# Optimization experiments

Measured on AMD Instinct MI355X. Metric: run time of the kernel, lower is better.

## Reference

```python
import jax, jax.numpy as jnp
import numpy as np

B, S, D = 4, 1024, 1024
H, HD = 16, 64
MAXPOS = 1024  # max_position_embeddings


def setup_inputs() -> dict:
    key = jax.random.key(0)
    ks = jax.random.split(key, 10)
    sc = 0.02
    return {
        "hidden_states": jax.random.normal(ks[0], (B, S, D), dtype=jnp.float32),
        "attention_mask": jnp.zeros((B, 1, 1, S), dtype=jnp.float32),
        "across_attention_prior": jax.random.uniform(ks[1], (B, H, S, S), dtype=jnp.float32),
        "head_mask": jnp.ones((1, H, 1, 1), dtype=jnp.float32),
        "Wq": jax.random.normal(ks[2], (D, D), dtype=jnp.float32) * sc,
        "bq": jnp.zeros((D,), dtype=jnp.float32),
        "Wk": jax.random.normal(ks[3], (D, D), dtype=jnp.float32) * sc,
        "bk": jnp.zeros((D,), dtype=jnp.float32),
        "Wv": jax.random.normal(ks[4], (D, D), dtype=jnp.float32) * sc,
        "bv": jnp.zeros((D,), dtype=jnp.float32),
        "dist_emb": jax.random.normal(ks[5], (2 * MAXPOS - 1, HD), dtype=jnp.float32) * sc,
    }


def _heads(x):
    # [B,S,D] -> [B,H,S,HD]
    return x.reshape(B, S, H, HD).transpose(0, 2, 1, 3)


def reference(hidden_states, attention_mask, across_attention_prior, head_mask,
              Wq, bq, Wk, bk, Wv, bv, dist_emb):
    q = _heads(hidden_states @ Wq + bq)  # [B,H,S,HD]
    k = _heads(hidden_states @ Wk + bk)
    v = _heads(hidden_states @ Wv + bv)

    scores = jnp.einsum("bhld,bhrd->bhlr", q, k)

    # relative_key_query positional bias
    pos = jnp.arange(S)
    distance = pos[:, None] - pos[None, :]  # [S,S]
    pe = dist_emb[distance + MAXPOS - 1]  # [S,S,HD] (l, r, d)
    scores = scores + jnp.einsum("bhld,lrd->bhlr", q, pe)
    scores = scores + jnp.einsum("bhrd,lrd->bhlr", k, pe)

    scores = scores / jnp.sqrt(jnp.float32(HD))
    scores = scores + attention_mask  # additive mask, broadcast [B,1,1,S]

    probs = jax.nn.softmax(scores, axis=-1)
    probs = probs * across_attention_prior  # post-softmax multiplicative prior
    probs = probs * head_mask  # dropout prob = 0 (eval)

    ctx = jnp.einsum("bhlr,bhrd->bhld", probs, v)
    ctx = ctx.transpose(0, 2, 1, 3).reshape(B, S, D)
    return ctx
```

## Files before the change

kernel.cpp:

```cpp
#include <hip/hip_runtime.h>


typedef unsigned short u16;
typedef unsigned int   u32;
typedef unsigned long long u64;
typedef __attribute__((ext_vector_type(8))) short bfx8;
typedef __attribute__((ext_vector_type(4))) float f32x4;

#define MFMA_BF16(a, b, c) __builtin_amdgcn_mfma_f32_16x16x32_bf16(a, b, c, 0, 0, 0)

__device__ __forceinline__ u16 f2bf(float f) {
    union { float f; u32 u; } c; c.f = f;
    u32 u = c.u;
    return (u16)((u + 0x7FFFu + ((u >> 16) & 1u)) >> 16);
}
__device__ __forceinline__ float bf2f(u16 v) {
    union { u32 u; float f; } c; c.u = ((u32)v) << 16;
    return c.f;
}
__device__ __forceinline__ float load_f(const void* p, long i, bool bf) {
    return bf ? bf2f(((const u16*)p)[i]) : ((const float*)p)[i];
}
__device__ __forceinline__ u16 load_bf(const void* p, long i, bool bf) {
    return bf ? ((const u16*)p)[i] : f2bf(((const float*)p)[i]);
}

__device__ __forceinline__ void gload16(const u16* g, u16* l) {
    __builtin_amdgcn_global_load_lds(
        (__attribute__((address_space(1))) void*)g,
        (__attribute__((address_space(3))) void*)l, 16, 0, 0);
}

__device__ __forceinline__ bfx8 ld_sw(const u16* arr, int row, int chunk) {
    return *(const bfx8*)(arr + row * 64 + ((chunk ^ (row & 7)) * 8));
}

__global__ void k_detect(const u32* hid, int* flags) {
    __shared__ int cnt;
    if (threadIdx.x == 0) cnt = 0;
    __syncthreads();
    int c = 0;
    for (int i = threadIdx.x; i < 1024; i += 256) {
        u32 w = hid[i];
        u32 e = (w >> 7) & 0xFFu;
        if (e >= 100u && e <= 140u) c++;
    }
    atomicAdd(&cnt, c);
    __syncthreads();
    if (threadIdx.x == 0) flags[0] = (cnt > 512) ? 1 : 0;
}

__global__ void k_prep(const void* hidden, const void* dist, const void* mask,
                       const void* hm, const void* bq, const void* bk,
                       const void* bv, const int* flags, u16* hid_bf,
                       u16* dist_bf, float* mask_f, float* hm_f, float* bias_f) {
    const bool bf = flags[0] != 0;
    const long NH = 4L * 1024 * 1024, ND = 2047L * 64, NM = 4096, NB = 3072, NHM = 16;
    const long TOT = NH + ND + NM + NB + NHM;
    for (long i = (long)blockIdx.x * 256 + threadIdx.x; i < TOT;
         i += (long)gridDim.x * 256) {
        if (i < NH) hid_bf[i] = load_bf(hidden, i, bf);
        else if (i < NH + ND) dist_bf[i - NH] = load_bf(dist, i - NH, bf);
        else if (i < NH + ND + NM) mask_f[i - NH - ND] = load_f(mask, i - NH - ND, bf);
        else if (i < NH + ND + NM + NB) {
            long j = i - NH - ND - NM;
            const void* src = (j < 1024) ? bq : ((j < 2048) ? bk : bv);
            bias_f[j] = load_f(src, j & 1023, bf);
        } else {
            long j = i - NH - ND - NM - NB;
            hm_f[j] = load_f(hm, j, bf);
        }
    }
}

__global__ void k_transpose(const void* Wq, const void* Wk, const void* Wv,
                            const int* flags, u16* wt) {
    const bool bf = flags[0] != 0;
    __shared__ float t[32][33];
    const int z = blockIdx.z;
    const void* W = (z == 0) ? Wq : ((z == 1) ? Wk : Wv);
    int x = blockIdx.x * 32 + threadIdx.x;
    for (int i = 0; i < 4; i++) {
        int y = blockIdx.y * 32 + threadIdx.y + i * 8;
        t[threadIdx.y + i * 8][threadIdx.x] = load_f(W, (long)y * 1024 + x, bf);
    }
    __syncthreads();
    int x2 = blockIdx.y * 32 + threadIdx.x;
    u16* out = wt + (long)z * 1024 * 1024;
    for (int i = 0; i < 4; i++) {
        int y2 = blockIdx.x * 32 + threadIdx.y + i * 8;
        out[(long)y2 * 1024 + x2] = f2bf(t[threadIdx.x][threadIdx.y + i * 8]);
    }
}

__global__ __launch_bounds__(256, 2)
void k_qkv_gemm(const u16* A, const u16* Bt, const float* bias,
                u16* qb, u16* kb, u16* vb) {
    __shared__ u16 sA[128 * 32];
    __shared__ u16 sB[128 * 32];
    const int tid = threadIdx.x;
    const int w = tid >> 6, lane = tid & 63;
    const int quad = lane >> 4, nl = lane & 15;
    const int wr = w >> 1, wc = w & 1;
    const int n0 = blockIdx.x * 128, m0 = blockIdx.y * 128;

    f32x4 acc[4][4];
#pragma unroll
    for (int a = 0; a < 4; a++)
#pragma unroll
        for (int b = 0; b < 4; b++) acc[a][b] = (f32x4){0.f, 0.f, 0.f, 0.f};

    for (int kt = 0; kt < 32; kt++) {
        const int k0 = kt * 32;
        __syncthreads();
#pragma unroll
        for (int j = 0; j < 2; j++) {
            int row = 32 * w + 16 * j + (lane >> 2);
            int seg = lane & 3;
            gload16(A + (long)(m0 + row) * 1024 + k0 + seg * 8, sA + 1024 * w + 512 * j);
            gload16(Bt + (long)(n0 + row) * 1024 + k0 + seg * 8, sB + 1024 * w + 512 * j);
        }
        __syncthreads();

        bfx8 af[4], bfr[4];
#pragma unroll
        for (int f = 0; f < 4; f++) {
            af[f]  = *(const bfx8*)(sA + (64 * wr + 16 * f + nl) * 32 + quad * 8);
            bfr[f] = *(const bfx8*)(sB + (64 * wc + 16 * f + nl) * 32 + quad * 8);
        }
#pragma unroll
        for (int fm = 0; fm < 4; fm++)
#pragma unroll
            for (int fn = 0; fn < 4; fn++)
                acc[fm][fn] = MFMA_BF16(af[fm], bfr[fn], acc[fm][fn]);
    }

#pragma unroll
    for (int fm = 0; fm < 4; fm++) {
#pragma unroll
        for (int fn = 0; fn < 4; fn++) {
            int n = n0 + 64 * wc + 16 * fn + nl;
            int which = n >> 10, hcol = n & 1023;
            int h = hcol >> 6, hd = hcol & 63;
            float bias_v = bias[n];
            int mbase = m0 + 64 * wr + 16 * fm + 4 * quad;
            int b = mbase >> 10, s = mbase & 1023;
            if (which == 2) {
                u64 pk = 0;
#pragma unroll
                for (int reg = 0; reg < 4; reg++)
                    pk |= (u64)f2bf(acc[fm][fn][reg] + bias_v) << (16 * reg);
                *(u64*)&vb[((long)((b * 16 + h) * 64 + hd)) * 1024 + s] = pk;
            } else {
                u16* op = (which == 0) ? qb : kb;
#pragma unroll
                for (int reg = 0; reg < 4; reg++)
                    op[((long)((b * 16 + h) * 1024 + s + reg)) * 64 + hd] =
                        f2bf(acc[fm][fn][reg] + bias_v);
            }
        }
    }
}

__global__ __launch_bounds__(256, 3)
void k_attn(const u16* qb, const u16* kb, const u16* vTb, const u16* Eb,
            const float* maskf, const float* hmf, const void* prior,
            const int* flags, void* out) {
    __shared__ __align__(16) u16 smem[25088];
    u16* sK  = smem;
    u16* sVT = smem + 4096;
    u16* sE  = smem + 8192;
    u16* sP  = smem + 8192;
    u16* bqB = smem + 16384;
    u16* bkB = smem + 20736;

    const int tid = threadIdx.x;
    const int w = tid >> 6, lane = tid & 63;
    const int quad = lane >> 4, nl = lane & 15;
    const int rloc = lane >> 3;
    const int cperm = (lane & 7) ^ rloc;
    const int bh = blockIdx.x, b = bh >> 4, h = bh & 15;
    const int l0 = blockIdx.y * 64;
    const bool bf = flags[0] != 0;

    const u16* qbh = qb  + (long)bh * 65536;
    const u16* kbh = kb  + (long)bh * 65536;
    const u16* vbh = vTb + (long)bh * 65536;

    const bfx8 aq0 = *(const bfx8*)(qbh + (l0 + 16 * w + nl) * 64 + quad * 8);
    const bfx8 aq1 = *(const bfx8*)(qbh + (l0 + 16 * w + nl) * 64 + quad * 8 + 32);

    f32x4 accv[4];
#pragma unroll
    for (int f = 0; f < 4; f++) accv[f] = (f32x4){0.f, 0.f, 0.f, 0.f};
    float zacc[4] = {0.f, 0.f, 0.f, 0.f};
    const int jb_base = l0 + 960;

    const int lpb   = 16 * w + 4 * quad;
    const int bqrd  = lpb * 68 + 63 - nl;
    const int bkrd  = lpb * 68 + nl;

    for (int it = 0; it < 16; it++) {
        const int r0 = it * 64;
        __syncthreads();

        const int jb = jb_base - r0;
#pragma unroll
        for (int j = 0; j < 2; j++) {
            int row = 16 * w + 8 * j + rloc;
            gload16(kbh + (r0 + row) * 64 + cperm * 8, sK + (16 * w + 8 * j) * 64);
            gload16(vbh + row * 1024 + r0 + cperm * 8, sVT + (16 * w + 8 * j) * 64);
        }
#pragma unroll
        for (int j = 0; j < 4; j++) {
            int row = 32 * w + 8 * j + rloc;
            int je = jb + row;
            if (je > 2046) je = 2046;
            if (je < 0) je = 0;
            gload16(Eb + je * 64 + cperm * 8, sE + (32 * w + 8 * j) * 64);
        }
        float pr[4][4], mval[4];
#pragma unroll
        for (int fn = 0; fn < 4; fn++) {
            mval[fn] = maskf[b * 1024 + r0 + fn * 16 + nl];
#pragma unroll
            for (int reg = 0; reg < 4; reg++) {
                long pidx = ((long)(bh * 1024 + l0 + 16 * w + 4 * quad + reg)) * 1024
                            + r0 + fn * 16 + nl;
                pr[fn][reg] = bf ? bf2f(((const u16*)prior)[pidx])
                                 : ((const float*)prior)[pidx];
            }
        }
        __syncthreads();

        const bfx8 ak0 = ld_sw(sK, 16 * w + nl, quad);
        const bfx8 ak1 = ld_sw(sK, 16 * w + nl, 4 + quad);
#pragma unroll
        for (int d = 0; d < 5; d++) {
            const int fc = w + d;
            bfx8 be0 = ld_sw(sE, fc * 16 + nl, quad);
            bfx8 be1 = ld_sw(sE, fc * 16 + nl, 4 + quad);
            f32x4 dq = (f32x4){0.f, 0.f, 0.f, 0.f};
            dq = MFMA_BF16(aq0, be0, dq);
            dq = MFMA_BF16(aq1, be1, dq);
#pragma unroll
            for (int reg = 0; reg < 4; reg++) {
                int lp = lpb + reg;
                int t = 16 * fc + nl - lp;
                if (t >= 0 && t < 64) bqB[lp * 68 + t] = f2bf(dq[reg]);
            }
        }
#pragma unroll
        for (int d = 0; d < 5; d++) {
            const int fc = 3 - w + d;
            bfx8 be0 = ld_sw(sE, fc * 16 + nl, quad);
            bfx8 be1 = ld_sw(sE, fc * 16 + nl, 4 + quad);
            f32x4 dk = (f32x4){0.f, 0.f, 0.f, 0.f};
            dk = MFMA_BF16(ak0, be0, dk);
            dk = MFMA_BF16(ak1, be1, dk);
#pragma unroll
            for (int reg = 0; reg < 4; reg++) {
                int rp = lpb + reg;
                int row = 16 * fc + nl + rp - 63;
                if (row >= 0 && row < 64) bkB[row * 68 + rp] = f2bf(dk[reg]);
            }
        }
        f32x4 accs[4];
#pragma unroll
        for (int fn = 0; fn < 4; fn++) {
            bfx8 bk0 = ld_sw(sK, fn * 16 + nl, quad);
            bfx8 bk1 = ld_sw(sK, fn * 16 + nl, 4 + quad);
            f32x4 s = (f32x4){0.f, 0.f, 0.f, 0.f};
            s = MFMA_BF16(aq0, bk0, s);
            s = MFMA_BF16(aq1, bk1, s);
            accs[fn] = s;
        }
        __syncthreads();

#pragma unroll
        for (int fn = 0; fn < 4; fn++) {
#pragma unroll
            for (int reg = 0; reg < 4; reg++) {
                float dqv = bf2f(bqB[bqrd + reg * 68 - fn * 16]);
                float dkv = bf2f(bkB[bkrd + reg * 68 + fn * 16]);
                float s = (accs[fn][reg] + dqv + dkv) * 0.125f + mval[fn];
                float e = __expf(s);
                zacc[reg] += e;
                sP[(lpb + reg) * 72 + fn * 16 + nl] = f2bf(e * pr[fn][reg]);
            }
        }
        bfx8 ap0 = *(const bfx8*)(sP + (16 * w + nl) * 72 + quad * 8);
        bfx8 ap1 = *(const bfx8*)(sP + (16 * w + nl) * 72 + quad * 8 + 32);
#pragma unroll
        for (int fd = 0; fd < 4; fd++) {
            bfx8 bv0 = ld_sw(sVT, fd * 16 + nl, quad);
            bfx8 bv1 = ld_sw(sVT, fd * 16 + nl, 4 + quad);
            accv[fd] = MFMA_BF16(ap0, bv0, accv[fd]);
            accv[fd] = MFMA_BF16(ap1, bv1, accv[fd]);
        }
    }

#pragma unroll
    for (int reg = 0; reg < 4; reg++) {
        float z = zacc[reg];
        z += __shfl_xor(z, 1);
        z += __shfl_xor(z, 2);
        z += __shfl_xor(z, 4);
        z += __shfl_xor(z, 8);
        zacc[reg] = z;
    }
    const float hm = hmf[h];
#pragma unroll
    for (int fd = 0; fd < 4; fd++) {
#pragma unroll
        for (int reg = 0; reg < 4; reg++) {
            int l = l0 + 16 * w + 4 * quad + reg;
            int d = fd * 16 + nl;
            float val = accv[fd][reg] * hm / zacc[reg];
            long oidx = ((long)(b * 1024 + l)) * 1024 + h * 64 + d;
            if (bf) ((u16*)out)[oidx] = f2bf(val);
            else    ((float*)out)[oidx] = val;
        }
    }
}

extern "C" void kernel_launch(void* const* d_in, const int* in_sizes, int n_in,
                              void* d_out, int out_size, void* d_ws, size_t ws_size,
                              hipStream_t stream) {
    char* ws = (char*)d_ws;
    int*   flags   = (int*)ws;
    u16*   hid_bf  = (u16*)(ws + 256);
    u16*   wt_bf   = (u16*)(ws + 8388864);
    u16*   dist_bf = (u16*)(ws + 14680320);
    float* mask_f  = (float*)(ws + 14942464);
    float* bias_f  = (float*)(ws + 14958848);
    float* hm_f    = (float*)(ws + 14971136);
    u16*   q_bf    = (u16*)(ws + 14971392);
    u16*   k_bf    = (u16*)(ws + 23360000);
    u16*   v_bf    = (u16*)(ws + 31748608);

    k_detect<<<1, 256, 0, stream>>>((const u32*)d_in[0], flags);
    k_prep<<<2048, 256, 0, stream>>>(d_in[0], d_in[10], d_in[1], d_in[3],
                                     d_in[5], d_in[7], d_in[9], flags,
                                     hid_bf, dist_bf, mask_f, hm_f, bias_f);
    k_transpose<<<dim3(32, 32, 3), dim3(32, 8), 0, stream>>>(
        d_in[4], d_in[6], d_in[8], flags, wt_bf);
    k_qkv_gemm<<<dim3(24, 32), 256, 0, stream>>>(hid_bf, wt_bf, bias_f,
                                                 q_bf, k_bf, v_bf);
    k_attn<<<dim3(64, 16), 256, 0, stream>>>(q_bf, k_bf, v_bf, dist_bf,
                                             mask_f, hm_f, d_in[2], flags, d_out);
}
```

Before: 521.9 us.

## Prefetch prior tiles one iteration ahead and stage K/V/E through registers

The attention kernel now loads the next iteration's prior and mask values into registers while the current tile is processed, so the large prior stream is meant to overlap with compute. K, V and E tiles are loaded into registers and stored to padded LDS rows (stride 72) in place of global_load_lds with XOR swizzle, and raw s_waitcnt+s_barrier sequences replace __syncthreads. The prep kernel converts hidden states and the distance table four elements per thread with vector loads and launches half as many blocks. The cost is higher register pressure from the doubled prior buffers and staging registers, which may reduce occupancy under launch bounds of 3 blocks per CU.

```diff
diff --git a/kernel.cpp b/kernel.cpp
--- a/kernel.cpp
+++ b/kernel.cpp
@@ -9,6 +9,9 @@
 
 #define MFMA_BF16(a, b, c) __builtin_amdgcn_mfma_f32_16x16x32_bf16(a, b, c, 0, 0, 0)
 
+#define BAR_LDS() asm volatile("s_waitcnt lgkmcnt(0)\n\ts_barrier" ::: "memory")
+#define CFENCE()  asm volatile("" ::: "memory")
+
 __device__ __forceinline__ u16 f2bf(float f) {
     union { float f; u32 u; } c; c.f = f;
     u32 u = c.u;
@@ -29,10 +32,6 @@
     __builtin_amdgcn_global_load_lds(
         (__attribute__((address_space(1))) void*)g,
         (__attribute__((address_space(3))) void*)l, 16, 0, 0);
-}
-
-__device__ __forceinline__ bfx8 ld_sw(const u16* arr, int row, int chunk) {
-    return *(const bfx8*)(arr + row * 64 + ((chunk ^ (row & 7)) * 8));
 }
 
 __global__ void k_detect(const u32* hid, int* flags) {
@@ -55,20 +54,32 @@
                        const void* bv, const int* flags, u16* hid_bf,
                        u16* dist_bf, float* mask_f, float* hm_f, float* bias_f) {
     const bool bf = flags[0] != 0;
-    const long NH = 4L * 1024 * 1024, ND = 2047L * 64, NM = 4096, NB = 3072, NHM = 16;
-    const long TOT = NH + ND + NM + NB + NHM;
+    const long VH = 1048576, VD = 32752;
+    const long SC = 4096 + 3072 + 16;
+    const long TOT = VH + VD + SC;
     for (long i = (long)blockIdx.x * 256 + threadIdx.x; i < TOT;
          i += (long)gridDim.x * 256) {
-        if (i < NH) hid_bf[i] = load_bf(hidden, i, bf);
-        else if (i < NH + ND) dist_bf[i - NH] = load_bf(dist, i - NH, bf);
-        else if (i < NH + ND + NM) mask_f[i - NH - ND] = load_f(mask, i - NH - ND, bf);
-        else if (i < NH + ND + NM + NB) {
-            long j = i - NH - ND - NM;
-            const void* src = (j < 1024) ? bq : ((j < 2048) ? bk : bv);
-            bias_f[j] = load_f(src, j & 1023, bf);
+        if (i < VH + VD) {
+            const void* src = (i < VH) ? hidden : dist;
+            u16* dst = (i < VH) ? hid_bf : dist_bf;
+            long j = (i < VH) ? i : i - VH;
+            if (bf) {
+                ((int2*)dst)[j] = ((const int2*)src)[j];
+            } else {
+                float4 v = ((const float4*)src)[j];
+                ushort4 o;
+                o.x = f2bf(v.x); o.y = f2bf(v.y);
+                o.z = f2bf(v.z); o.w = f2bf(v.w);
+                ((ushort4*)dst)[j] = o;
+            }
         } else {
-            long j = i - NH - ND - NM - NB;
-            hm_f[j] = load_f(hm, j, bf);
+            long j = i - VH - VD;
+            if (j < 4096) mask_f[j] = load_f(mask, j, bf);
+            else if (j < 7168) {
+                long k = j - 4096;
+                const void* src = (k < 1024) ? bq : ((k < 2048) ? bk : bv);
+                bias_f[k] = load_f(src, k & 1023, bf);
+            } else hm_f[j - 7168] = load_f(hm, j - 7168, bf);
         }
     }
 }
@@ -166,19 +177,17 @@
 void k_attn(const u16* qb, const u16* kb, const u16* vTb, const u16* Eb,
             const float* maskf, const float* hmf, const void* prior,
             const int* flags, void* out) {
-    __shared__ __align__(16) u16 smem[25088];
+    __shared__ __align__(16) u16 smem[27136];
     u16* sK  = smem;
-    u16* sVT = smem + 4096;
-    u16* sE  = smem + 8192;
-    u16* sP  = smem + 8192;
-    u16* bqB = smem + 16384;
-    u16* bkB = smem + 20736;
+    u16* sVT = smem + 4608;
+    u16* sE  = smem + 9216;
+    u16* sP  = smem + 9216;
+    u16* bqB = smem + 18432;
+    u16* bkB = smem + 22784;
 
     const int tid = threadIdx.x;
     const int w = tid >> 6, lane = tid & 63;
     const int quad = lane >> 4, nl = lane & 15;
-    const int rloc = lane >> 3;
-    const int cperm = (lane & 7) ^ rloc;
     const int bh = blockIdx.x, b = bh >> 4, h = bh & 15;
     const int l0 = blockIdx.y * 64;
     const bool bf = flags[0] != 0;
@@ -196,50 +205,79 @@
     float zacc[4] = {0.f, 0.f, 0.f, 0.f};
     const int jb_base = l0 + 960;
 
-    const int lpb   = 16 * w + 4 * quad;
-    const int bqrd  = lpb * 68 + 63 - nl;
-    const int bkrd  = lpb * 68 + nl;
-
+    const int lpb  = 16 * w + 4 * quad;
+    const int bqrd = lpb * 68 + 63 - nl;
+    const int bkrd = lpb * 68 + nl;
+
+    float pr_c[4][4], mv_c[4], pr_n[4][4], mv_n[4];
+#pragma unroll
+    for (int fn = 0; fn < 4; fn++) {
+        mv_c[fn] = maskf[b * 1024 + fn * 16 + nl];
+#pragma unroll
+        for (int reg = 0; reg < 4; reg++) {
+            long pidx = ((long)(bh * 1024 + l0 + lpb + reg)) * 1024 + fn * 16 + nl;
+            pr_c[fn][reg] = bf ? bf2f(((const u16*)prior)[pidx])
+                               : ((const float*)prior)[pidx];
+        }
+    }
+
+#pragma unroll 2
     for (int it = 0; it < 16; it++) {
         const int r0 = it * 64;
-        __syncthreads();
-
+        BAR_LDS();
+
+        int4 vKr[2], vVr[2], vEr[4];
+#pragma unroll
+        for (int p = 0; p < 2; p++) {
+            int cid = tid + 256 * p, row = cid >> 3, c8 = cid & 7;
+            vKr[p] = *(const int4*)(kbh + (r0 + row) * 64 + c8 * 8);
+            vVr[p] = *(const int4*)(vbh + row * 1024 + r0 + c8 * 8);
+        }
         const int jb = jb_base - r0;
 #pragma unroll
-        for (int j = 0; j < 2; j++) {
-            int row = 16 * w + 8 * j + rloc;
-            gload16(kbh + (r0 + row) * 64 + cperm * 8, sK + (16 * w + 8 * j) * 64);
-            gload16(vbh + row * 1024 + r0 + cperm * 8, sVT + (16 * w + 8 * j) * 64);
-        }
-#pragma unroll
-        for (int j = 0; j < 4; j++) {
-            int row = 32 * w + 8 * j + rloc;
+        for (int p = 0; p < 4; p++) {
+            int cid = tid + 256 * p, row = cid >> 3, c8 = cid & 7;
             int je = jb + row;
-            if (je > 2046) je = 2046;
-            if (je < 0) je = 0;
-            gload16(Eb + je * 64 + cperm * 8, sE + (32 * w + 8 * j) * 64);
-        }
-        float pr[4][4], mval[4];
-#pragma unroll
-        for (int fn = 0; fn < 4; fn++) {
-            mval[fn] = maskf[b * 1024 + r0 + fn * 16 + nl];
-#pragma unroll
-            for (int reg = 0; reg < 4; reg++) {
-                long pidx = ((long)(bh * 1024 + l0 + 16 * w + 4 * quad + reg)) * 1024
-                            + r0 + fn * 16 + nl;
-                pr[fn][reg] = bf ? bf2f(((const u16*)prior)[pidx])
-                                 : ((const float*)prior)[pidx];
-            }
-        }
-        __syncthreads();
-
-        const bfx8 ak0 = ld_sw(sK, 16 * w + nl, quad);
-        const bfx8 ak1 = ld_sw(sK, 16 * w + nl, 4 + quad);
+            je = je < 0 ? 0 : (je > 2046 ? 2046 : je);
+            vEr[p] = *(const int4*)(Eb + je * 64 + c8 * 8);
+        }
+        CFENCE();
+        {
+            const int itn = it < 15 ? it + 1 : it;
+            const int r0n = itn * 64;
+#pragma unroll
+            for (int fn = 0; fn < 4; fn++) {
+                mv_n[fn] = maskf[b * 1024 + r0n + fn * 16 + nl];
+#pragma unroll
+                for (int reg = 0; reg < 4; reg++) {
+                    long pidx = ((long)(bh * 1024 + l0 + lpb + reg)) * 1024
+                                + r0n + fn * 16 + nl;
+                    pr_n[fn][reg] = bf ? bf2f(((const u16*)prior)[pidx])
+                                       : ((const float*)prior)[pidx];
+                }
+            }
+        }
+        CFENCE();
+#pragma unroll
+        for (int p = 0; p < 2; p++) {
+            int cid = tid + 256 * p, row = cid >> 3, c8 = cid & 7;
+            *(int4*)(sK  + row * 72 + c8 * 8) = vKr[p];
+            *(int4*)(sVT + row * 72 + c8 * 8) = vVr[p];
+        }
+#pragma unroll
+        for (int p = 0; p < 4; p++) {
+            int cid = tid + 256 * p, row = cid >> 3, c8 = cid & 7;
+            *(int4*)(sE + row * 72 + c8 * 8) = vEr[p];
+        }
+        BAR_LDS();
+
+        const bfx8 ak0 = *(const bfx8*)(sK + (16 * w + nl) * 72 + quad * 8);
+        const bfx8 ak1 = *(const bfx8*)(sK + (16 * w + nl) * 72 + quad * 8 + 32);
 #pragma unroll
         for (int d = 0; d < 5; d++) {
             const int fc = w + d;
-            bfx8 be0 = ld_sw(sE, fc * 16 + nl, quad);
-            bfx8 be1 = ld_sw(sE, fc * 16 + nl, 4 + quad);
+            bfx8 be0 = *(const bfx8*)(sE + (fc * 16 + nl) * 72 + quad * 8);
+            bfx8 be1 = *(const bfx8*)(sE + (fc * 16 + nl) * 72 + quad * 8 + 32);
             f32x4 dq = (f32x4){0.f, 0.f, 0.f, 0.f};
             dq = MFMA_BF16(aq0, be0, dq);
             dq = MFMA_BF16(aq1, be1, dq);
@@ -253,8 +291,8 @@
 #pragma unroll
         for (int d = 0; d < 5; d++) {
             const int fc = 3 - w + d;
-            bfx8 be0 = ld_sw(sE, fc * 16 + nl, quad);
-            bfx8 be1 = ld_sw(sE, fc * 16 + nl, 4 + quad);
+            bfx8 be0 = *(const bfx8*)(sE + (fc * 16 + nl) * 72 + quad * 8);
+            bfx8 be1 = *(const bfx8*)(sE + (fc * 16 + nl) * 72 + quad * 8 + 32);
             f32x4 dk = (f32x4){0.f, 0.f, 0.f, 0.f};
             dk = MFMA_BF16(ak0, be0, dk);
             dk = MFMA_BF16(ak1, be1, dk);
@@ -268,14 +306,14 @@
         f32x4 accs[4];
 #pragma unroll
         for (int fn = 0; fn < 4; fn++) {
-            bfx8 bk0 = ld_sw(sK, fn * 16 + nl, quad);
-            bfx8 bk1 = ld_sw(sK, fn * 16 + nl, 4 + quad);
+            bfx8 bk0 = *(const bfx8*)(sK + (fn * 16 + nl) * 72 + quad * 8);
+            bfx8 bk1 = *(const bfx8*)(sK + (fn * 16 + nl) * 72 + quad * 8 + 32);
             f32x4 s = (f32x4){0.f, 0.f, 0.f, 0.f};
             s = MFMA_BF16(aq0, bk0, s);
             s = MFMA_BF16(aq1, bk1, s);
             accs[fn] = s;
         }
-        __syncthreads();
+        BAR_LDS();
 
 #pragma unroll
         for (int fn = 0; fn < 4; fn++) {
@@ -283,20 +321,26 @@
             for (int reg = 0; reg < 4; reg++) {
                 float dqv = bf2f(bqB[bqrd + reg * 68 - fn * 16]);
                 float dkv = bf2f(bkB[bkrd + reg * 68 + fn * 16]);
-                float s = (accs[fn][reg] + dqv + dkv) * 0.125f + mval[fn];
+                float s = (accs[fn][reg] + dqv + dkv) * 0.125f + mv_c[fn];
                 float e = __expf(s);
                 zacc[reg] += e;
-                sP[(lpb + reg) * 72 + fn * 16 + nl] = f2bf(e * pr[fn][reg]);
+                sP[(lpb + reg) * 72 + fn * 16 + nl] = f2bf(e * pr_c[fn][reg]);
             }
         }
         bfx8 ap0 = *(const bfx8*)(sP + (16 * w + nl) * 72 + quad * 8);
         bfx8 ap1 = *(const bfx8*)(sP + (16 * w + nl) * 72 + quad * 8 + 32);
 #pragma unroll
         for (int fd = 0; fd < 4; fd++) {
-            bfx8 bv0 = ld_sw(sVT, fd * 16 + nl, quad);
-            bfx8 bv1 = ld_sw(sVT, fd * 16 + nl, 4 + quad);
+            bfx8 bv0 = *(const bfx8*)(sVT + (fd * 16 + nl) * 72 + quad * 8);
+            bfx8 bv1 = *(const bfx8*)(sVT + (fd * 16 + nl) * 72 + quad * 8 + 32);
             accv[fd] = MFMA_BF16(ap0, bv0, accv[fd]);
             accv[fd] = MFMA_BF16(ap1, bv1, accv[fd]);
+        }
+#pragma unroll
+        for (int fn = 0; fn < 4; fn++) {
+            mv_c[fn] = mv_n[fn];
+#pragma unroll
+            for (int reg = 0; reg < 4; reg++) pr_c[fn][reg] = pr_n[fn][reg];
         }
     }
 
@@ -340,7 +384,7 @@
     u16*   v_bf    = (u16*)(ws + 31748608);
 
     k_detect<<<1, 256, 0, stream>>>((const u32*)d_in[0], flags);
-    k_prep<<<2048, 256, 0, stream>>>(d_in[0], d_in[10], d_in[1], d_in[3],
+    k_prep<<<1024, 256, 0, stream>>>(d_in[0], d_in[10], d_in[1], d_in[3],
                                      d_in[5], d_in[7], d_in[9], flags,
                                      hid_bf, dist_bf, mask_f, hm_f, bias_f);
     k_transpose<<<dim3(32, 32, 3), dim3(32, 8), 0, stream>>>(
```

New measurement: 906.7 us. 1.74x slower.
